# Kernel tuning notes

Hardware: AMD Instinct MI355X
Metric: run time of the kernel (lower is better)

The kernel has to match this reference:

```python
import jax, jax.numpy as jnp
import numpy as np

ALPHA = 4.0  # spikingjelly surrogate.Sigmoid default
V_TH = 1.0

@jax.custom_vjp
def spike_fn(x):
    # Heaviside: spike when membrane potential crosses threshold (x = v - V_TH)
    return (x >= 0.0).astype(x.dtype)

def _spike_fwd(x):
    return spike_fn(x), x

def _spike_bwd(x, g):
    s = jax.nn.sigmoid(ALPHA * x)
    return (g * ALPHA * s * (1.0 - s),)

spike_fn.defvjp(_spike_fwd, _spike_bwd)

def setup_inputs() -> dict:
    key = jax.random.key(0)
    k1, k2 = jax.random.split(key)
    T, B, F, O = 64, 2048, 784, 10
    x_spike = jax.random.uniform(k1, (T, B, F), dtype=jnp.float32)
    W = jax.random.normal(k2, (O, F), dtype=jnp.float32) * (1.0 / np.sqrt(F))
    b = jnp.zeros((O,), dtype=jnp.float32)
    return {"x_spike": x_spike, "W": W, "b": b}

def reference(x_spike, W, b):
    T, B, _ = x_spike.shape
    O = W.shape[0]

    def step(v, xt):
        c = jnp.dot(xt, W.T) + b              # [B, O] synaptic current
        v = v + c                              # IF neuron charge
        s = spike_fn(v - V_TH)                 # fire
        v = v * (1.0 - s)                      # hard reset to v_reset=0 (non-detached)
        return v, s

    v0 = jnp.zeros((B, O), dtype=x_spike.dtype)
    _, spikes = jax.lax.scan(step, v0, x_spike)  # spikes: [T, B, O]
    return spikes.mean(axis=0)                   # firing-rate output
```

## Files before the change

### kernel.cpp

```cpp
#include <hip/hip_runtime.h>


#define T_STEPS 64
#define BATCH   2048
#define FEAT    784
#define OUT_N   10
#define ROWS    (T_STEPS * BATCH)

typedef __attribute__((ext_vector_type(4))) float f4;
typedef __attribute__((ext_vector_type(2))) float f2;

template <int CTRL>
__device__ __forceinline__ float dpp_mov(float v) {
    return __int_as_float(
        __builtin_amdgcn_update_dpp(0, __float_as_int(v), CTRL, 0xF, 0xF, true));
}
__device__ __forceinline__ float red16(float v) {
    v += dpp_mov<0xB1>(v);
    v += dpp_mov<0x4E>(v);
    v += dpp_mov<0x141>(v);
    v += dpp_mov<0x140>(v);
    return v;
}

__global__ __launch_bounds__(256)
void snn_gemm(const float* __restrict__ x, const float* __restrict__ W,
              const float* __restrict__ bias, float* __restrict__ C) {
    __shared__ float Wl[OUT_N * FEAT];

    {
        const f4* Wg = (const f4*)W;
        f4* Ws = (f4*)Wl;
        for (int i = threadIdx.x; i < OUT_N * FEAT / 4; i += 256) Ws[i] = Wg[i];
    }
    __syncthreads();

    const int tid  = threadIdx.x;
    const int w    = tid >> 6;
    const int ln   = tid & 63;
    const int l16  = ln & 15;
    const int r    = ln >> 4;
    const long row0 = (long)blockIdx.x * 64 + w * 16 + r * 4;

    const float* xbase = x + (size_t)row0 * FEAT + 4 * l16;

    float acc[4][OUT_N];
#pragma unroll
    for (int g = 0; g < 4; ++g)
#pragma unroll
        for (int o = 0; o < OUT_N; ++o) acc[g][o] = 0.0f;

    f4 cur[4];
#pragma unroll
    for (int g = 0; g < 4; ++g)
        cur[g] = *(const f4*)(xbase + (size_t)g * FEAT);

#pragma unroll 2
    for (int c = 0; c < 12; ++c) {
        f4 nxt[4];
        if (c < 11) {
#pragma unroll
            for (int g = 0; g < 4; ++g)
                nxt[g] = *(const f4*)(xbase + (size_t)g * FEAT + (c + 1) * 64);
        }
#pragma unroll
        for (int o = 0; o < OUT_N; ++o) {
            const f4 wf = *(const f4*)&Wl[o * FEAT + c * 64 + l16 * 4];
#pragma unroll
            for (int g = 0; g < 4; ++g) {
                acc[g][o] = fmaf(cur[g].x, wf.x, acc[g][o]);
                acc[g][o] = fmaf(cur[g].y, wf.y, acc[g][o]);
                acc[g][o] = fmaf(cur[g].z, wf.z, acc[g][o]);
                acc[g][o] = fmaf(cur[g].w, wf.w, acc[g][o]);
            }
        }
        if (c < 11) {
#pragma unroll
            for (int g = 0; g < 4; ++g) cur[g] = nxt[g];
        }
    }

    if (l16 < 4) {
#pragma unroll
        for (int g = 0; g < 4; ++g) {
            const f4 xt = *(const f4*)(xbase + (size_t)g * FEAT + 768);
#pragma unroll
            for (int o = 0; o < OUT_N; ++o) {
                const f4 wf = *(const f4*)&Wl[o * FEAT + 768 + l16 * 4];
                acc[g][o] = fmaf(xt.x, wf.x, acc[g][o]);
                acc[g][o] = fmaf(xt.y, wf.y, acc[g][o]);
                acc[g][o] = fmaf(xt.z, wf.z, acc[g][o]);
                acc[g][o] = fmaf(xt.w, wf.w, acc[g][o]);
            }
        }
    }

#pragma unroll
    for (int g = 0; g < 4; ++g)
#pragma unroll
        for (int o = 0; o < OUT_N; ++o) acc[g][o] = red16(acc[g][o]);

    if (l16 == 0) {
#pragma unroll
        for (int g = 0; g < 4; ++g) {
            float* Cr = C + (size_t)(row0 + g) * OUT_N;
#pragma unroll
            for (int p = 0; p < 5; ++p) {
                f2 s;
                s.x = acc[g][2 * p]     + bias[2 * p];
                s.y = acc[g][2 * p + 1] + bias[2 * p + 1];
                *(f2*)&Cr[2 * p] = s;
            }
        }
    }
}

__global__ __launch_bounds__(256)
void snn_scan(const float* __restrict__ C, float* __restrict__ out) {
    const int idx = blockIdx.x * 256 + threadIdx.x;
    if (idx >= BATCH * OUT_N) return;
    float v = 0.0f;
    float cnt = 0.0f;
#pragma unroll
    for (int t = 0; t < T_STEPS; ++t) {
        v += C[(size_t)t * BATCH * OUT_N + idx];
        if (v >= 1.0f) { cnt += 1.0f; v = 0.0f; }
    }
    out[idx] = cnt * (1.0f / 64.0f);
}

extern "C" void kernel_launch(void* const* d_in, const int* in_sizes, int n_in,
                              void* d_out, int out_size, void* d_ws, size_t ws_size,
                              hipStream_t stream) {
    const float* x    = (const float*)d_in[0];
    const float* W    = (const float*)d_in[1];
    const float* bias = (const float*)d_in[2];
    float* out = (float*)d_out;
    float* C   = (float*)d_ws;

    snn_gemm<<<dim3(ROWS / 64), dim3(256), 0, stream>>>(x, W, bias, C);
    snn_scan<<<dim3((BATCH * OUT_N + 255) / 256), dim3(256), 0, stream>>>(C, out);
}
```

Measured before the change: 88.30 us.

## Map whole wavefront across each row and process rows in four passes

Each wavefront now owns 16 rows, handled in four passes of four rows. All 64 lanes span the 768-float body of a row, so each lane issues 12 vector loads up front. The 16-float tail is handled by lane groups, and results are reduced across the full wave with DPP, swizzle and shuffle before four lanes store the rows. This aims to raise memory-level parallelism and make row reads contiguous across the wave, at the cost of four times more cross-lane reductions and no prefetch across passes.

```diff
diff --git a/kernel.cpp b/kernel.cpp
--- a/kernel.cpp
+++ b/kernel.cpp
@@ -22,6 +22,12 @@
     v += dpp_mov<0x140>(v);
     return v;
 }
+__device__ __forceinline__ float red64(float v) {
+    v = red16(v);
+    v += __int_as_float(__builtin_amdgcn_ds_swizzle(__float_as_int(v), 0x401F));
+    v += __shfl_xor(v, 32, 64);
+    return v;
+}
 
 __global__ __launch_bounds__(256)
 void snn_gemm(const float* __restrict__ x, const float* __restrict__ W,
@@ -38,80 +44,84 @@
     const int tid  = threadIdx.x;
     const int w    = tid >> 6;
     const int ln   = tid & 63;
-    const int l16  = ln & 15;
-    const int r    = ln >> 4;
-    const long row0 = (long)blockIdx.x * 64 + w * 16 + r * 4;
+    const int wgid = blockIdx.x * 4 + w;
 
-    const float* xbase = x + (size_t)row0 * FEAT + 4 * l16;
+    f2 bv[5];
+#pragma unroll
+    for (int p = 0; p < 5; ++p) { bv[p].x = bias[2 * p]; bv[p].y = bias[2 * p + 1]; }
 
-    float acc[4][OUT_N];
+    const int gsel = ln >> 4;
+    const int tq   = ln & 15;
+
+#pragma unroll 1
+    for (int p = 0; p < 4; ++p) {
+        const long row0 = (long)wgid * 16 + p * 4;
+        const float* xr0 = x + (size_t)row0 * FEAT;
+
+        f4 xr[4][3];
 #pragma unroll
-    for (int g = 0; g < 4; ++g)
+        for (int g = 0; g < 4; ++g)
 #pragma unroll
-        for (int o = 0; o < OUT_N; ++o) acc[g][o] = 0.0f;
+            for (int c = 0; c < 3; ++c)
+                xr[g][c] = *(const f4*)(xr0 + (size_t)g * FEAT + c * 256 + ln * 4);
+        f4 xt = {0.0f, 0.0f, 0.0f, 0.0f};
+        if (tq < 4)
+            xt = *(const f4*)(xr0 + (size_t)gsel * FEAT + 768 + tq * 4);
 
-    f4 cur[4];
+        float acc[4][OUT_N];
 #pragma unroll
-    for (int g = 0; g < 4; ++g)
-        cur[g] = *(const f4*)(xbase + (size_t)g * FEAT);
+        for (int g = 0; g < 4; ++g)
+#pragma unroll
+            for (int o = 0; o < OUT_N; ++o) acc[g][o] = 0.0f;
 
-#pragma unroll 2
-    for (int c = 0; c < 12; ++c) {
-        f4 nxt[4];
-        if (c < 11) {
 #pragma unroll
-            for (int g = 0; g < 4; ++g)
-                nxt[g] = *(const f4*)(xbase + (size_t)g * FEAT + (c + 1) * 64);
-        }
+        for (int c = 0; c < 3; ++c)
+#pragma unroll
+            for (int o = 0; o < OUT_N; ++o) {
+                const f4 wf = *(const f4*)&Wl[o * FEAT + c * 256 + ln * 4];
+#pragma unroll
+                for (int g = 0; g < 4; ++g) {
+                    acc[g][o] = fmaf(xr[g][c].x, wf.x, acc[g][o]);
+                    acc[g][o] = fmaf(xr[g][c].y, wf.y, acc[g][o]);
+                    acc[g][o] = fmaf(xr[g][c].z, wf.z, acc[g][o]);
+                    acc[g][o] = fmaf(xr[g][c].w, wf.w, acc[g][o]);
+                }
+            }
+
 #pragma unroll
         for (int o = 0; o < OUT_N; ++o) {
-            const f4 wf = *(const f4*)&Wl[o * FEAT + c * 64 + l16 * 4];
-#pragma unroll
-            for (int g = 0; g < 4; ++g) {
-                acc[g][o] = fmaf(cur[g].x, wf.x, acc[g][o]);
-                acc[g][o] = fmaf(cur[g].y, wf.y, acc[g][o]);
-                acc[g][o] = fmaf(cur[g].z, wf.z, acc[g][o]);
-                acc[g][o] = fmaf(cur[g].w, wf.w, acc[g][o]);
-            }
+            const f4 wt = *(const f4*)&Wl[o * FEAT + 768 + (ln & 3) * 4];
+            float s = xt.x * wt.x;
+            s = fmaf(xt.y, wt.y, s);
+            s = fmaf(xt.z, wt.z, s);
+            s = fmaf(xt.w, wt.w, s);
+            acc[0][o] += (gsel == 0) ? s : 0.0f;
+            acc[1][o] += (gsel == 1) ? s : 0.0f;
+            acc[2][o] += (gsel == 2) ? s : 0.0f;
+            acc[3][o] += (gsel == 3) ? s : 0.0f;
         }
-        if (c < 11) {
-#pragma unroll
-            for (int g = 0; g < 4; ++g) cur[g] = nxt[g];
-        }
-    }
-
-    if (l16 < 4) {
-#pragma unroll
-        for (int g = 0; g < 4; ++g) {
-            const f4 xt = *(const f4*)(xbase + (size_t)g * FEAT + 768);
-#pragma unroll
-            for (int o = 0; o < OUT_N; ++o) {
-                const f4 wf = *(const f4*)&Wl[o * FEAT + 768 + l16 * 4];
-                acc[g][o] = fmaf(xt.x, wf.x, acc[g][o]);
-                acc[g][o] = fmaf(xt.y, wf.y, acc[g][o]);
-                acc[g][o] = fmaf(xt.z, wf.z, acc[g][o]);
-                acc[g][o] = fmaf(xt.w, wf.w, acc[g][o]);
-            }
-        }
-    }
 
 #pragma unroll
-    for (int g = 0; g < 4; ++g)
+        for (int g = 0; g < 4; ++g)
 #pragma unroll
-        for (int o = 0; o < OUT_N; ++o) acc[g][o] = red16(acc[g][o]);
+            for (int o = 0; o < OUT_N; ++o) acc[g][o] = red64(acc[g][o]);
 
-    if (l16 == 0) {
-#pragma unroll
-        for (int g = 0; g < 4; ++g) {
-            float* Cr = C + (size_t)(row0 + g) * OUT_N;
-#pragma unroll
-            for (int p = 0; p < 5; ++p) {
-                f2 s;
-                s.x = acc[g][2 * p]     + bias[2 * p];
-                s.y = acc[g][2 * p + 1] + bias[2 * p + 1];
-                *(f2*)&Cr[2 * p] = s;
-            }
-        }
+#define STORE_ROW(G)                                                      \
+        do {                                                              \
+            float* Cr = C + (size_t)(row0 + (G)) * OUT_N;                 \
+            _Pragma("unroll")                                             \
+            for (int q = 0; q < 5; ++q) {                                 \
+                f2 s;                                                     \
+                s.x = acc[(G)][2 * q]     + bv[q].x;                      \
+                s.y = acc[(G)][2 * q + 1] + bv[q].y;                      \
+                *(f2*)&Cr[2 * q] = s;                                     \
+            }                                                             \
+        } while (0)
+        if      (ln == 0) STORE_ROW(0);
+        else if (ln == 1) STORE_ROW(1);
+        else if (ln == 2) STORE_ROW(2);
+        else if (ln == 3) STORE_ROW(3);
+#undef STORE_ROW
     }
 }
 
```

After: 131.0 us. 48.3% more time.

## Fuse GEMM and IF-neuron scan into one kernel, one block per batch item

Applied to the files above, without the earlier changes.

Each block now handles one batch element across all 64 timesteps. It keeps the per-timestep currents in shared memory and runs the threshold/reset scan inside the block. This removes the second kernel launch and the global round-trip through the workspace C buffer. The cost is that the x rows a block reads are now strided by B*F rather than contiguous, and only 10 threads do the serial scan at the end of each block.

```diff
diff --git a/kernel.cpp b/kernel.cpp
--- a/kernel.cpp
+++ b/kernel.cpp
@@ -5,7 +5,6 @@
 #define BATCH   2048
 #define FEAT    784
 #define OUT_N   10
-#define ROWS    (T_STEPS * BATCH)
 
 typedef __attribute__((ext_vector_type(4))) float f4;
 typedef __attribute__((ext_vector_type(2))) float f2;
@@ -24,9 +23,10 @@
 }
 
 __global__ __launch_bounds__(256)
-void snn_gemm(const float* __restrict__ x, const float* __restrict__ W,
-              const float* __restrict__ bias, float* __restrict__ C) {
+void snn_fused(const float* __restrict__ x, const float* __restrict__ W,
+               const float* __restrict__ bias, float* __restrict__ out) {
     __shared__ float Wl[OUT_N * FEAT];
+    __shared__ float part[T_STEPS * OUT_N];
 
     {
         const f4* Wg = (const f4*)W;
@@ -35,14 +35,16 @@
     }
     __syncthreads();
 
-    const int tid  = threadIdx.x;
-    const int w    = tid >> 6;
-    const int ln   = tid & 63;
-    const int l16  = ln & 15;
-    const int r    = ln >> 4;
-    const long row0 = (long)blockIdx.x * 64 + w * 16 + r * 4;
+    const int tid = threadIdx.x;
+    const int w   = tid >> 6;
+    const int ln  = tid & 63;
+    const int l16 = ln & 15;
+    const int r   = ln >> 4;
+    const int b   = blockIdx.x;
+    const int t0  = w * 16 + r * 4;
 
-    const float* xbase = x + (size_t)row0 * FEAT + 4 * l16;
+    const float* xbase = x + ((size_t)t0 * BATCH + b) * FEAT + 4 * l16;
+    const size_t gstr  = (size_t)BATCH * FEAT;
 
     float acc[4][OUT_N];
 #pragma unroll
@@ -53,7 +55,7 @@
     f4 cur[4];
 #pragma unroll
     for (int g = 0; g < 4; ++g)
-        cur[g] = *(const f4*)(xbase + (size_t)g * FEAT);
+        cur[g] = *(const f4*)(xbase + gstr * g);
 
 #pragma unroll 2
     for (int c = 0; c < 12; ++c) {
@@ -61,7 +63,7 @@
         if (c < 11) {
 #pragma unroll
             for (int g = 0; g < 4; ++g)
-                nxt[g] = *(const f4*)(xbase + (size_t)g * FEAT + (c + 1) * 64);
+                nxt[g] = *(const f4*)(xbase + gstr * g + (c + 1) * 64);
         }
 #pragma unroll
         for (int o = 0; o < OUT_N; ++o) {
@@ -83,7 +85,7 @@
     if (l16 < 4) {
 #pragma unroll
         for (int g = 0; g < 4; ++g) {
-            const f4 xt = *(const f4*)(xbase + (size_t)g * FEAT + 768);
+            const f4 xt = *(const f4*)(xbase + gstr * g + 768);
 #pragma unroll
             for (int o = 0; o < OUT_N; ++o) {
                 const f4 wf = *(const f4*)&Wl[o * FEAT + 768 + l16 * 4];
@@ -103,30 +105,30 @@
     if (l16 == 0) {
 #pragma unroll
         for (int g = 0; g < 4; ++g) {
-            float* Cr = C + (size_t)(row0 + g) * OUT_N;
+            float* p = &part[(t0 + g) * OUT_N];
 #pragma unroll
-            for (int p = 0; p < 5; ++p) {
+            for (int q = 0; q < 5; ++q) {
                 f2 s;
-                s.x = acc[g][2 * p]     + bias[2 * p];
-                s.y = acc[g][2 * p + 1] + bias[2 * p + 1];
-                *(f2*)&Cr[2 * p] = s;
+                s.x = acc[g][2 * q];
+                s.y = acc[g][2 * q + 1];
+                *(f2*)&p[2 * q] = s;
             }
         }
     }
-}
+    __syncthreads();
 
-__global__ __launch_bounds__(256)
-void snn_scan(const float* __restrict__ C, float* __restrict__ out) {
-    const int idx = blockIdx.x * 256 + threadIdx.x;
-    if (idx >= BATCH * OUT_N) return;
-    float v = 0.0f;
-    float cnt = 0.0f;
+    if (tid < OUT_N) {
+        const float bo = bias[tid];
+        float v = 0.0f, cnt = 0.0f;
 #pragma unroll
-    for (int t = 0; t < T_STEPS; ++t) {
-        v += C[(size_t)t * BATCH * OUT_N + idx];
-        if (v >= 1.0f) { cnt += 1.0f; v = 0.0f; }
+        for (int t = 0; t < T_STEPS; ++t) {
+            const float vv = v + part[t * OUT_N + tid] + bo;
+            const bool  s  = (vv >= 1.0f);
+            cnt += s ? 1.0f : 0.0f;
+            v = s ? 0.0f : vv;
+        }
+        out[b * OUT_N + tid] = cnt * (1.0f / 64.0f);
     }
-    out[idx] = cnt * (1.0f / 64.0f);
 }
 
 extern "C" void kernel_launch(void* const* d_in, const int* in_sizes, int n_in,
@@ -136,8 +138,6 @@
     const float* W    = (const float*)d_in[1];
     const float* bias = (const float*)d_in[2];
     float* out = (float*)d_out;
-    float* C   = (float*)d_ws;
 
-    snn_gemm<<<dim3(ROWS / 64), dim3(256), 0, stream>>>(x, W, bias, C);
-    snn_scan<<<dim3((BATCH * OUT_N + 255) / 256), dim3(256), 0, stream>>>(C, out);
+    snn_fused<<<dim3(BATCH), dim3(256), 0, stream>>>(x, W, bias, out);
 }
```

New measurement: 87.76 us. About the same (-0.6%).
